# Performance work log

Measured on AMD Instinct MI355X. Metric: run time of the kernel, lower is better.

Reference implementation:

```python
import jax, jax.numpy as jnp
import numpy as np

N = 100_000   # nodes
E = 1_600_000 # edges (avg degree 16)
D = 128       # input_dim
H = 128       # hidden_dim
G = 64        # graphs in batch
C = 2         # num_classes


def setup_inputs() -> dict:
    key = jax.random.key(0)
    ks = jax.random.split(key, 16)
    x = jax.random.normal(ks[0], (N, D), dtype=jnp.float32)
    edge_index = jax.random.randint(ks[1], (2, E), 0, N, dtype=jnp.int32)
    batch = jnp.sort(jax.random.randint(ks[2], (N,), 0, G, dtype=jnp.int32))
    def lin(k, fin, fout):
        s = 1.0 / np.sqrt(fin)
        kw, kb = jax.random.split(k)
        W = jax.random.uniform(kw, (fin, fout), jnp.float32, -s, s)
        b = jax.random.uniform(kb, (fout,), jnp.float32, -s, s)
        return W, b
    W0, b0 = lin(ks[3], D, H)
    W1, b1 = lin(ks[4], H, H)
    W2, b2 = lin(ks[5], H, H)
    Wc1, bc1 = lin(ks[6], 2 * H, H)
    Wc2, bc2 = lin(ks[7], H, C)
    return dict(x=x, edge_index=edge_index, batch=batch,
                W0=W0, b0=b0, W1=W1, b1=b1, W2=W2, b2=b2,
                Wc1=Wc1, bc1=bc1, Wc2=Wc2, bc2=bc2)


def _gcn_layer(x, W, b, src, dst, dinv):
    # GCNConv with self-loops and symmetric normalization:
    # out_i = sum_{j->i} d_j^{-1/2} d_i^{-1/2} (x_j W) + d_i^{-1} (x_i W) + b
    h = x @ W                                   # [N, H]
    coef = dinv[src] * dinv[dst]                # [E]
    agg = jax.ops.segment_sum(h[src] * coef[:, None], dst, num_segments=N)
    return agg + h * (dinv * dinv)[:, None] + b


def reference(x, edge_index, batch, W0, b0, W1, b1, W2, b2, Wc1, bc1, Wc2, bc2):
    src, dst = edge_index[0], edge_index[1]
    # degree with self-loops (in-degree on target nodes + 1)
    deg = jax.ops.segment_sum(jnp.ones((E,), jnp.float32), dst, num_segments=N) + 1.0
    dinv = jax.lax.rsqrt(deg)
    for W, b in ((W0, b0), (W1, b1), (W2, b2)):
        x = jax.nn.relu(_gcn_layer(x, W, b, src, dst, dinv))
        # dropout: inference mode -> identity
    # global mean pool per graph
    sums = jax.ops.segment_sum(x, batch, num_segments=G)            # [G, H]
    cnt = jax.ops.segment_sum(jnp.ones((N,), jnp.float32), batch, num_segments=G)
    pooled = sums / jnp.maximum(cnt, 1.0)[:, None]
    combined = jnp.concatenate([pooled, pooled], axis=1)            # [G, 2H]
    hcls = jax.nn.relu(combined @ Wc1 + bc1)
    return hcls @ Wc2 + bc2                                         # [G, C]
```

## Files before the change

### kernel.cpp

```cpp
#include <hip/hip_runtime.h>

#define HDIM 128
#define GCOUNT 64
#define CHUNK 2048

__device__ __forceinline__ float bfl(unsigned u) { return __uint_as_float(u << 16); }
__device__ __forceinline__ float bfh(unsigned u) { return __uint_as_float(u & 0xffff0000u); }
__device__ __forceinline__ unsigned short f2bf(float f) {
  unsigned u = __float_as_uint(f);
  unsigned r = (u + 0x7fffu + ((u >> 16) & 1u)) >> 16;
  return (unsigned short)r;
}
__device__ __forceinline__ unsigned pk2(float a, float b) {
  return (unsigned)f2bf(a) | ((unsigned)f2bf(b) << 16);
}

typedef __attribute__((ext_vector_type(8))) short short8;
typedef __attribute__((ext_vector_type(4))) float f32x4;

__device__ __forceinline__ unsigned qb(float v, float rinv) {
  int q = (int)rintf(v * rinv);
  return (unsigned)(q & 0xff);
}


__global__ void mega1(const float* __restrict__ W0, const float* __restrict__ W1,
                      const float* __restrict__ W2,
                      unsigned short* __restrict__ h0, unsigned short* __restrict__ l0,
                      unsigned short* __restrict__ h1, unsigned short* __restrict__ l1,
                      unsigned short* __restrict__ h2, unsigned short* __restrict__ l2,
                      float* __restrict__ pooled, float* __restrict__ gcnt, int pz,
                      const int* __restrict__ dst, int E, int G, int NB1,
                      int* __restrict__ gcount,
                      const float* __restrict__ x, uint2* __restrict__ S,
                      float* __restrict__ cs_base, int n) {
  __shared__ int hist[512];
  int b = blockIdx.x, t = threadIdx.x;
  if (b < 192) {
    int w = b >> 6;
    int idx = (b & 63) * 256 + t;
    const float* W = (w == 0) ? W0 : (w == 1) ? W1 : W2;
    unsigned short* hi = (w == 0) ? h0 : (w == 1) ? h1 : h2;
    unsigned short* lo = (w == 0) ? l0 : (w == 1) ? l1 : l2;
    int k = idx >> 7, nn = idx & 127;
    float wv = W[idx];
    unsigned short h = f2bf(wv);
    float hf = __uint_as_float((unsigned)h << 16);
    unsigned short l = f2bf(wv - hf);
    hi[nn * 128 + k] = h;
    lo[nn * 128 + k] = l;
  } else if (b < 192 + pz) {
    int i = (b - 192) * 256 + t;
    if (i < GCOUNT * HDIM) pooled[i] = 0.f;
    else if (i - GCOUNT * HDIM < GCOUNT) gcnt[i - GCOUNT * HDIM] = 0.f;
  } else if (b < 192 + pz + G) {
    int blk = b - 192 - pz;
    for (int i = t; i < NB1; i += 256) hist[i] = 0;
    __syncthreads();
    int base = blk * CHUNK;
    #pragma unroll
    for (int j = 0; j < CHUNK / 256; j++) {
      int e = base + j * 256 + t;
      if (e < E) atomicAdd(&hist[dst[e] >> 8], 1);
    }
    __syncthreads();
    for (int i = t; i < NB1; i += 256) gcount[i * G + blk] = hist[i];
  } else {
    int idx = (b - 192 - pz - G) * 16 + (t >> 4);
    int l = t & 15;
    int ridx = min(idx, n - 1);
    float4 f0 = ((const float4*)x)[(size_t)ridx * 32 + l * 2];
    float4 f1 = ((const float4*)x)[(size_t)ridx * 32 + l * 2 + 1];
    float v0 = f0.x, v1 = f0.y, v2 = f0.z, v3 = f0.w;
    float v4 = f1.x, v5 = f1.y, v6 = f1.z, v7 = f1.w;
    float mx = fmaxf(fmaxf(fmaxf(fabsf(v0), fabsf(v1)), fmaxf(fabsf(v2), fabsf(v3))),
                     fmaxf(fmaxf(fabsf(v4), fabsf(v5)), fmaxf(fabsf(v6), fabsf(v7))));
    mx = fmaxf(mx, __shfl_xor(mx, 1));
    mx = fmaxf(mx, __shfl_xor(mx, 2));
    mx = fmaxf(mx, __shfl_xor(mx, 4));
    mx = fmaxf(mx, __shfl_xor(mx, 8));
    float c = mx * (1.0f / 127.0f);
    float rinv = (mx > 0.f) ? 127.0f / mx : 0.f;
    if (idx < n) {
      unsigned lo = qb(v0, rinv) | (qb(v1, rinv) << 8) | (qb(v2, rinv) << 16) | (qb(v3, rinv) << 24);
      unsigned hi = qb(v4, rinv) | (qb(v5, rinv) << 8) | (qb(v6, rinv) << 16) | (qb(v7, rinv) << 24);
      S[(size_t)idx * 16 + l] = make_uint2(lo, hi);
      if (l == 0) cs_base[idx] = c;
    }
  }
}


__global__ void scanA(int* __restrict__ g, int* __restrict__ bsum, int M) {
  __shared__ int sh[1024];
  int t = threadIdx.x;
  int i = blockIdx.x * 1024 + t;
  int v = (i < M) ? g[i] : 0;
  sh[t] = v;
  __syncthreads();
  for (int off = 1; off < 1024; off <<= 1) {
    int u = (t >= off) ? sh[t - off] : 0;
    __syncthreads();
    sh[t] += u;
    __syncthreads();
  }
  if (i < M) g[i] = sh[t] - v;
  if (t == 1023) bsum[blockIdx.x] = sh[1023];
}

__global__ void scanB(int* __restrict__ g, const int* __restrict__ bsum, int nb, int M) {
  __shared__ int sh[512];
  int t = threadIdx.x;
  if (t < 512) sh[t] = (t < nb) ? bsum[t] : 0;
  __syncthreads();
  for (int off = 1; off < 512; off <<= 1) {
    int u = (t < 512 && t >= off) ? sh[t - off] : 0;
    __syncthreads();
    if (t < 512) sh[t] += u;
    __syncthreads();
  }
  #pragma unroll
  for (int k = 0; k < 2; k++) {
    int i = blockIdx.x * 2048 + k * 1024 + t;
    if (i < M) {
      int j = i >> 10;
      if (j) g[i] += sh[j - 1];
    }
  }
}


__global__ void rs_scatter(const int* __restrict__ src, const int* __restrict__ dst,
                           const int* __restrict__ gscan, int E, int G, int NB1,
                           uint2* __restrict__ sp) {
  __shared__ int run[512];
  int blk = blockIdx.x, t = threadIdx.x;
  for (int i = t; i < NB1; i += 256) run[i] = gscan[i * G + blk];
  __syncthreads();
  int base = blk * CHUNK;
  #pragma unroll
  for (int j = 0; j < CHUNK / 256; j++) {
    int e = base + j * 256 + t;
    if (e < E) {
      int d = dst[e];
      int pos = atomicAdd(&run[d >> 8], 1);
      sp[pos] = make_uint2((unsigned)d, (unsigned)src[e]);
    }
  }
}


__global__ void csr_fine(const uint2* __restrict__ sp, const int* __restrict__ gscan,
                         int E, int G, int NB1,
                         int* __restrict__ rowp, int* __restrict__ colv,
                         float* __restrict__ dinv, const float* __restrict__ cs_base,
                         float* __restrict__ cs, int n) {
  __shared__ int hist[256];
  __shared__ int scn[256];
  __shared__ int run2[256];
  int hb = blockIdx.x, t = threadIdx.x;
  int O = gscan[hb * G];
  int Oe = (hb == NB1 - 1) ? E : gscan[(hb + 1) * G];
  if (t < 256) hist[t] = 0;
  __syncthreads();
  for (int e = O + t; e < Oe; e += 512) atomicAdd(&hist[sp[e].x & 255], 1);
  __syncthreads();
  int v = 0;
  if (t < 256) { v = hist[t]; scn[t] = v; }
  __syncthreads();
  for (int off = 1; off < 256; off <<= 1) {
    int u = (t < 256 && t >= off) ? scn[t - off] : 0;
    __syncthreads();
    if (t < 256) scn[t] += u;
    __syncthreads();
  }
  if (t < 256) {
    int excl = scn[t] - v;
    run2[t] = O + excl;
    int d = (hb << 8) + t;
    rowp[d] = O + excl;
    if (d < n) {
      float dv = rsqrtf((float)v + 1.0f);
      dinv[d] = dv;
      cs[d] = cs_base[d] * dv;
    }
  }
  if (hb == NB1 - 1 && t == 0) rowp[n] = E;
  __syncthreads();
  for (int e = O + t; e < Oe; e += 512) {
    uint2 p = sp[e];
    int pos = atomicAdd(&run2[p.x & 255], 1);
    colv[pos] = (int)p.y;
  }
}


__device__ __forceinline__ void acc8(uint2 v, float c, float* a) {
  int xx = (int)v.x, yy = (int)v.y;
  a[0] += c * (float)(signed char)(xx);
  a[1] += c * (float)(signed char)(xx >> 8);
  a[2] += c * (float)(signed char)(xx >> 16);
  a[3] += c * (float)(xx >> 24);
  a[4] += c * (float)(signed char)(yy);
  a[5] += c * (float)(signed char)(yy >> 8);
  a[6] += c * (float)(signed char)(yy >> 16);
  a[7] += c * (float)(yy >> 24);
}

__global__ void agg_i8(const uint2* __restrict__ S, const float* __restrict__ cs,
                       const float* __restrict__ dinv,
                       const int* __restrict__ rowp, const int* __restrict__ col,
                       uint4* __restrict__ OUT, int n) {
  int g = (blockIdx.x * blockDim.x + threadIdx.x) >> 4;
  int lane = threadIdx.x & 15;
  if (g >= n) return;
  float a[8];
  {
    uint2 q = S[(size_t)g * 16 + lane];
    float c = cs[g];
    int xx = (int)q.x, yy = (int)q.y;
    a[0] = c * (float)(signed char)(xx);
    a[1] = c * (float)(signed char)(xx >> 8);
    a[2] = c * (float)(signed char)(xx >> 16);
    a[3] = c * (float)(xx >> 24);
    a[4] = c * (float)(signed char)(yy);
    a[5] = c * (float)(signed char)(yy >> 8);
    a[6] = c * (float)(signed char)(yy >> 16);
    a[7] = c * (float)(yy >> 24);
  }
  int e0 = rowp[g], e1 = rowp[g + 1];
  int e = e0;
  for (; e + 7 < e1; e += 8) {
    int s0 = col[e],     s1 = col[e + 1], s2 = col[e + 2], s3 = col[e + 3];
    int s4 = col[e + 4], s5 = col[e + 5], s6 = col[e + 6], s7 = col[e + 7];
    uint2 q0 = S[(size_t)s0 * 16 + lane];
    uint2 q1 = S[(size_t)s1 * 16 + lane];
    uint2 q2 = S[(size_t)s2 * 16 + lane];
    uint2 q3 = S[(size_t)s3 * 16 + lane];
    uint2 q4 = S[(size_t)s4 * 16 + lane];
    uint2 q5 = S[(size_t)s5 * 16 + lane];
    uint2 q6 = S[(size_t)s6 * 16 + lane];
    uint2 q7 = S[(size_t)s7 * 16 + lane];
    float c0 = cs[s0], c1 = cs[s1], c2 = cs[s2], c3 = cs[s3];
    float c4 = cs[s4], c5 = cs[s5], c6 = cs[s6], c7 = cs[s7];
    acc8(q0, c0, a); acc8(q1, c1, a); acc8(q2, c2, a); acc8(q3, c3, a);
    acc8(q4, c4, a); acc8(q5, c5, a); acc8(q6, c6, a); acc8(q7, c7, a);
  }
  for (; e + 3 < e1; e += 4) {
    int s0 = col[e], s1 = col[e + 1], s2 = col[e + 2], s3 = col[e + 3];
    uint2 q0 = S[(size_t)s0 * 16 + lane];
    uint2 q1 = S[(size_t)s1 * 16 + lane];
    uint2 q2 = S[(size_t)s2 * 16 + lane];
    uint2 q3 = S[(size_t)s3 * 16 + lane];
    float c0 = cs[s0], c1 = cs[s1], c2 = cs[s2], c3 = cs[s3];
    acc8(q0, c0, a); acc8(q1, c1, a); acc8(q2, c2, a); acc8(q3, c3, a);
  }
  for (; e < e1; e++) {
    int s = col[e];
    uint2 q = S[(size_t)s * 16 + lane];
    acc8(q, cs[s], a);
  }
  float d = dinv[g];
  uint4 o;
  o.x = pk2(a[0] * d, a[1] * d); o.y = pk2(a[2] * d, a[3] * d);
  o.z = pk2(a[4] * d, a[5] * d); o.w = pk2(a[6] * d, a[7] * d);
  OUT[(size_t)g * 16 + lane] = o;
}


__global__ __launch_bounds__(256) void gemm_mfma_q8(
    const uint4* __restrict__ A, const uint4* __restrict__ WThi, const uint4* __restrict__ WTlo,
    const float* __restrict__ bias, const float* __restrict__ dinv,
    unsigned char* __restrict__ Sout, float* __restrict__ csout, int n) {
  __shared__ char smem[34816];
  __shared__ float Lc[64];
  uint4* Wl = (uint4*)smem;
  int t = threadIdx.x;
  int lane = t & 63, wv = t >> 6;
  int m = lane & 15, quad = lane >> 4;
  int block0 = blockIdx.x * 64;
  int arow = block0 + wv * 16 + m;
  uint4 av[4];
  #pragma unroll
  for (int kb = 0; kb < 4; kb++)
    av[kb] = (arow < n) ? A[(size_t)arow * 16 + kb * 4 + quad] : make_uint4(0, 0, 0, 0);
  f32x4 acc[8];
  #pragma unroll
  for (int i = 0; i < 8; i++) acc[i] = (f32x4){0.f, 0.f, 0.f, 0.f};

  #pragma unroll
  for (int i = 0; i < 8; i++) {
    int idx = t + i * 256;
    Wl[(idx >> 4) * 17 + (idx & 15)] = WThi[idx];
  }
  __syncthreads();
  #pragma unroll
  for (int kb = 0; kb < 4; kb++) {
    short8 af = __builtin_bit_cast(short8, av[kb]);
    #pragma unroll
    for (int nt = 0; nt < 8; nt++) {
      uint4 bh = Wl[(nt * 16 + m) * 17 + kb * 4 + quad];
      acc[nt] = __builtin_amdgcn_mfma_f32_16x16x32_bf16(af, __builtin_bit_cast(short8, bh), acc[nt], 0, 0, 0);
    }
  }
  __syncthreads();
  #pragma unroll
  for (int i = 0; i < 8; i++) {
    int idx = t + i * 256;
    Wl[(idx >> 4) * 17 + (idx & 15)] = WTlo[idx];
  }
  __syncthreads();
  #pragma unroll
  for (int kb = 0; kb < 4; kb++) {
    short8 af = __builtin_bit_cast(short8, av[kb]);
    #pragma unroll
    for (int nt = 0; nt < 8; nt++) {
      uint4 bl = Wl[(nt * 16 + m) * 17 + kb * 4 + quad];
      acc[nt] = __builtin_amdgcn_mfma_f32_16x16x32_bf16(af, __builtin_bit_cast(short8, bl), acc[nt], 0, 0, 0);
    }
  }
  __syncthreads();

  #pragma unroll
  for (int r = 0; r < 4; r++) {
    int lrow = wv * 16 + quad * 4 + r;
    int grow = block0 + lrow;
    float sc = (grow < n) ? dinv[grow] : 0.f;
    float v[8];
    float mx = 0.f;
    #pragma unroll
    for (int nt = 0; nt < 8; nt++) {
      v[nt] = fmaxf(acc[nt][r] + bias[nt * 16 + m], 0.f) * sc;
      mx = fmaxf(mx, v[nt]);
    }
    mx = fmaxf(mx, __shfl_xor(mx, 1));
    mx = fmaxf(mx, __shfl_xor(mx, 2));
    mx = fmaxf(mx, __shfl_xor(mx, 4));
    mx = fmaxf(mx, __shfl_xor(mx, 8));
    float c = mx * (1.0f / 127.0f);
    float rinv = (mx > 0.f) ? 127.0f / mx : 0.f;
    #pragma unroll
    for (int nt = 0; nt < 8; nt++) {
      smem[lrow * 144 + nt * 16 + m] = (char)(int)rintf(v[nt] * rinv);
    }
    if (m == 0) Lc[lrow] = c;
  }
  __syncthreads();
  for (int i = t; i < 512; i += 256) {
    int lrow = i >> 3, seg = i & 7;
    int grow = block0 + lrow;
    if (grow < n)
      ((uint4*)Sout)[(size_t)grow * 8 + seg] = *(const uint4*)&smem[lrow * 144 + seg * 16];
  }
  if (t < 64 && block0 + t < n) csout[block0 + t] = Lc[t];
}


__global__ __launch_bounds__(256) void gemm_mfma(
    const uint4* __restrict__ A, const uint4* __restrict__ WThi, const uint4* __restrict__ WTlo,
    const float* __restrict__ bias, unsigned short* __restrict__ Y, int n) {
  __shared__ char smem[34816];
  uint4* Wl = (uint4*)smem;
  int t = threadIdx.x;
  int lane = t & 63, wv = t >> 6;
  int m = lane & 15, quad = lane >> 4;
  int block0 = blockIdx.x * 64;
  int arow = block0 + wv * 16 + m;
  uint4 av[4];
  #pragma unroll
  for (int kb = 0; kb < 4; kb++)
    av[kb] = (arow < n) ? A[(size_t)arow * 16 + kb * 4 + quad] : make_uint4(0, 0, 0, 0);
  f32x4 acc[8];
  #pragma unroll
  for (int i = 0; i < 8; i++) acc[i] = (f32x4){0.f, 0.f, 0.f, 0.f};

  #pragma unroll
  for (int i = 0; i < 8; i++) {
    int idx = t + i * 256;
    Wl[(idx >> 4) * 17 + (idx & 15)] = WThi[idx];
  }
  __syncthreads();
  #pragma unroll
  for (int kb = 0; kb < 4; kb++) {
    short8 af = __builtin_bit_cast(short8, av[kb]);
    #pragma unroll
    for (int nt = 0; nt < 8; nt++) {
      uint4 bh = Wl[(nt * 16 + m) * 17 + kb * 4 + quad];
      acc[nt] = __builtin_amdgcn_mfma_f32_16x16x32_bf16(af, __builtin_bit_cast(short8, bh), acc[nt], 0, 0, 0);
    }
  }
  __syncthreads();
  #pragma unroll
  for (int i = 0; i < 8; i++) {
    int idx = t + i * 256;
    Wl[(idx >> 4) * 17 + (idx & 15)] = WTlo[idx];
  }
  __syncthreads();
  #pragma unroll
  for (int kb = 0; kb < 4; kb++) {
    short8 af = __builtin_bit_cast(short8, av[kb]);
    #pragma unroll
    for (int nt = 0; nt < 8; nt++) {
      uint4 bl = Wl[(nt * 16 + m) * 17 + kb * 4 + quad];
      acc[nt] = __builtin_amdgcn_mfma_f32_16x16x32_bf16(af, __builtin_bit_cast(short8, bl), acc[nt], 0, 0, 0);
    }
  }
  __syncthreads();

  unsigned short* Ls = (unsigned short*)smem;
  #pragma unroll
  for (int r = 0; r < 4; r++) {
    int lrow = wv * 16 + quad * 4 + r;
    #pragma unroll
    for (int nt = 0; nt < 8; nt++) {
      float v = fmaxf(acc[nt][r] + bias[nt * 16 + m], 0.f);
      Ls[lrow * 136 + nt * 16 + m] = f2bf(v);
    }
  }
  __syncthreads();
  for (int i = t; i < 1024; i += 256) {
    int lrow = i >> 4, seg = i & 15;
    int grow = block0 + lrow;
    if (grow < n)
      ((uint4*)Y)[(size_t)grow * 16 + seg] = *(const uint4*)&smem[lrow * 272 + seg * 16];
  }
}


__global__ void pool_kernel(const unsigned short* __restrict__ X, const int* __restrict__ batch,
                            float* __restrict__ pooled, float* __restrict__ gcnt, int n) {
  int t = threadIdx.x;
  int r0 = blockIdx.x * 64;
  if (r0 >= n) return;
  int r1 = min(r0 + 64, n);
  int g = batch[r0];
  float acc = 0.f, cl = 0.f;
  for (int r = r0; r < r1; r++) {
    int gr = batch[r];
    if (gr != g) {
      atomicAdd(&pooled[g * HDIM + t], acc);
      if (t == 0) atomicAdd(&gcnt[g], cl);
      acc = 0.f; cl = 0.f; g = gr;
    }
    acc += __uint_as_float((unsigned)X[(size_t)r * HDIM + t] << 16);
    cl += 1.f;
  }
  atomicAdd(&pooled[g * HDIM + t], acc);
  if (t == 0) atomicAdd(&gcnt[g], cl);
}


__global__ void cls_kernel(const float* __restrict__ pooled, const float* __restrict__ gcnt,
                           const float* __restrict__ Wc1, const float* __restrict__ bc1,
                           const float* __restrict__ Wc2, const float* __restrict__ bc2,
                           float* __restrict__ out) {
  __shared__ float p[HDIM];
  __shared__ float r0s[HDIM], r1s[HDIM];
  int g = blockIdx.x, t = threadIdx.x;
  float c = fmaxf(gcnt[g], 1.0f);
  p[t] = pooled[g * HDIM + t] / c;
  __syncthreads();
  float acc = bc1[t];
  for (int k = 0; k < HDIM; k++) {
    acc += p[k] * (Wc1[k * HDIM + t] + Wc1[(HDIM + k) * HDIM + t]);
  }
  float h = fmaxf(acc, 0.f);
  r0s[t] = h * Wc2[t * 2 + 0];
  r1s[t] = h * Wc2[t * 2 + 1];
  __syncthreads();
  for (int s2 = 64; s2 > 0; s2 >>= 1) {
    if (t < s2) { r0s[t] += r0s[t + s2]; r1s[t] += r1s[t + s2]; }
    __syncthreads();
  }
  if (t == 0) {
    out[g * 2 + 0] = r0s[0] + bc2[0];
    out[g * 2 + 1] = r1s[0] + bc2[1];
  }
}


extern "C" void kernel_launch(void* const* d_in, const int* in_sizes, int n_in,
                              void* d_out, int out_size, void* d_ws, size_t ws_size,
                              hipStream_t stream) {
  const float* x   = (const float*)d_in[0];
  const int*   ei  = (const int*)d_in[1];
  const int*   bat = (const int*)d_in[2];
  const float* W0  = (const float*)d_in[3];
  const float* b0  = (const float*)d_in[4];
  const float* W1  = (const float*)d_in[5];
  const float* b1  = (const float*)d_in[6];
  const float* W2  = (const float*)d_in[7];
  const float* b2  = (const float*)d_in[8];
  const float* Wc1 = (const float*)d_in[9];
  const float* bc1 = (const float*)d_in[10];
  const float* Wc2 = (const float*)d_in[11];
  const float* bc2 = (const float*)d_in[12];
  float* out = (float*)d_out;

  int N = in_sizes[0] / HDIM;
  int E = in_sizes[1] / 2;
  const int* src = ei;
  const int* dst = ei + E;

  int NB1 = (N + 255) >> 8;
  int G = (E + CHUNK - 1) / CHUNK;
  int M = NB1 * G;

  char* ws = (char*)d_ws;
  size_t off = 0;
  auto alloc = [&](size_t bytes) -> void* {
    void* p = (void*)(ws + off);
    off += (bytes + 511) & ~(size_t)511;
    return p;
  };
  unsigned char* Sa = (unsigned char*)alloc((size_t)N * HDIM * 2);
  unsigned char* Sb = Sa + (size_t)N * HDIM;
  unsigned short* H = (unsigned short*)Sa;
  unsigned short* Abuf = (unsigned short*)alloc((size_t)N * HDIM * 2);
  float* csa  = (float*)alloc((size_t)N * 4);
  float* csb  = (float*)alloc((size_t)N * 4);
  float* cs_base = (float*)alloc((size_t)N * 4);
  float* dinv = (float*)alloc((size_t)N * 4);
  int*   rowp = (int*)alloc((size_t)(NB1 * 256 + 2) * 4);
  int*   colv = (int*)alloc((size_t)E * 4);
  uint2* sp   = (uint2*)alloc((size_t)E * 8);
  float* pooled = (float*)alloc((size_t)GCOUNT * HDIM * 4);
  float* gcnt   = (float*)alloc((size_t)GCOUNT * 4);
  unsigned short* wt_hi[3], *wt_lo[3];
  for (int i = 0; i < 3; i++) {
    wt_hi[i] = (unsigned short*)alloc(HDIM * HDIM * 2);
    wt_lo[i] = (unsigned short*)alloc(HDIM * HDIM * 2);
  }
  int* gcount = (int*)alloc((size_t)(M + 2) * 4);
  int nbM = (M + 1023) / 1024;
  int* bsum = (int*)alloc((size_t)nbM * 4);

  int pz = (GCOUNT * HDIM + GCOUNT + 255) / 256;
  int psb = (N + 15) / 16;
  mega1<<<192 + pz + G + psb, 256, 0, stream>>>(W0, W1, W2,
      wt_hi[0], wt_lo[0], wt_hi[1], wt_lo[1], wt_hi[2], wt_lo[2],
      pooled, gcnt, pz, dst, E, G, NB1, gcount,
      x, (uint2*)Sa, cs_base, N);

  scanA<<<nbM, 1024, 0, stream>>>(gcount, bsum, M);
  scanB<<<(M + 2047) / 2048, 1024, 0, stream>>>(gcount, bsum, nbM, M);

  rs_scatter<<<G, 256, 0, stream>>>(src, dst, gcount, E, G, NB1, sp);
  csr_fine<<<NB1, 512, 0, stream>>>(sp, gcount, E, G, NB1, rowp, colv,
      dinv, cs_base, csa, N);

  int aggBlocks = (N + 15) / 16;
  int gemmBlocks = (N + 63) / 64;

  agg_i8<<<aggBlocks, 256, 0, stream>>>((const uint2*)Sa, csa, dinv, rowp, colv, (uint4*)Abuf, N);
  gemm_mfma_q8<<<gemmBlocks, 256, 0, stream>>>((const uint4*)Abuf, (const uint4*)wt_hi[0],
      (const uint4*)wt_lo[0], b0, dinv, Sb, csb, N);

  agg_i8<<<aggBlocks, 256, 0, stream>>>((const uint2*)Sb, csb, dinv, rowp, colv, (uint4*)Abuf, N);
  gemm_mfma_q8<<<gemmBlocks, 256, 0, stream>>>((const uint4*)Abuf, (const uint4*)wt_hi[1],
      (const uint4*)wt_lo[1], b1, dinv, Sa, csa, N);

  agg_i8<<<aggBlocks, 256, 0, stream>>>((const uint2*)Sa, csa, dinv, rowp, colv, (uint4*)Abuf, N);
  gemm_mfma<<<gemmBlocks, 256, 0, stream>>>((const uint4*)Abuf, (const uint4*)wt_hi[2],
      (const uint4*)wt_lo[2], b2, H, N);

  pool_kernel<<<(N + 63) / 64, 128, 0, stream>>>(H, bat, pooled, gcnt, N);
  cls_kernel<<<GCOUNT, HDIM, 0, stream>>>(pooled, gcnt, Wc1, bc1, Wc2, bc2, out);
}
```

Baseline: 378.7 us.

## Fuse int8 aggregation with MFMA GEMM and pooling into per-layer kernels

Each layer's int8 neighbour aggregation now runs inside the GEMM kernel. The aggregated bf16 tile goes straight into shared memory in MFMA operand layout, so the Abuf round-trip through global memory and one launch per layer are gone. The last layer also folds the mean-pool atomics into the epilogue instead of writing H and running a separate pool kernel. Blocks grow to 512 threads covering 128 rows with 64 KB of shared memory, and weight staging uses an MFMA-friendly layout overlapped with the aggregation. The cost is lower occupancy and less latency hiding for the gather-heavy aggregation, since each 16-lane group now handles 4 rows serially.

```diff
diff --git a/kernel.cpp b/kernel.cpp
--- a/kernel.cpp
+++ b/kernel.cpp
@@ -207,120 +207,135 @@
   a[7] += c * (float)(yy >> 24);
 }
 
-__global__ void agg_i8(const uint2* __restrict__ S, const float* __restrict__ cs,
-                       const float* __restrict__ dinv,
-                       const int* __restrict__ rowp, const int* __restrict__ col,
-                       uint4* __restrict__ OUT, int n) {
-  int g = (blockIdx.x * blockDim.x + threadIdx.x) >> 4;
-  int lane = threadIdx.x & 15;
-  if (g >= n) return;
-  float a[8];
-  {
-    uint2 q = S[(size_t)g * 16 + lane];
-    float c = cs[g];
-    int xx = (int)q.x, yy = (int)q.y;
-    a[0] = c * (float)(signed char)(xx);
-    a[1] = c * (float)(signed char)(xx >> 8);
-    a[2] = c * (float)(signed char)(xx >> 16);
-    a[3] = c * (float)(xx >> 24);
-    a[4] = c * (float)(signed char)(yy);
-    a[5] = c * (float)(signed char)(yy >> 8);
-    a[6] = c * (float)(signed char)(yy >> 16);
-    a[7] = c * (float)(yy >> 24);
-  }
-  int e0 = rowp[g], e1 = rowp[g + 1];
-  int e = e0;
-  for (; e + 7 < e1; e += 8) {
-    int s0 = col[e],     s1 = col[e + 1], s2 = col[e + 2], s3 = col[e + 3];
-    int s4 = col[e + 4], s5 = col[e + 5], s6 = col[e + 6], s7 = col[e + 7];
-    uint2 q0 = S[(size_t)s0 * 16 + lane];
-    uint2 q1 = S[(size_t)s1 * 16 + lane];
-    uint2 q2 = S[(size_t)s2 * 16 + lane];
-    uint2 q3 = S[(size_t)s3 * 16 + lane];
-    uint2 q4 = S[(size_t)s4 * 16 + lane];
-    uint2 q5 = S[(size_t)s5 * 16 + lane];
-    uint2 q6 = S[(size_t)s6 * 16 + lane];
-    uint2 q7 = S[(size_t)s7 * 16 + lane];
-    float c0 = cs[s0], c1 = cs[s1], c2 = cs[s2], c3 = cs[s3];
-    float c4 = cs[s4], c5 = cs[s5], c6 = cs[s6], c7 = cs[s7];
-    acc8(q0, c0, a); acc8(q1, c1, a); acc8(q2, c2, a); acc8(q3, c3, a);
-    acc8(q4, c4, a); acc8(q5, c5, a); acc8(q6, c6, a); acc8(q7, c7, a);
-  }
-  for (; e + 3 < e1; e += 4) {
-    int s0 = col[e], s1 = col[e + 1], s2 = col[e + 2], s3 = col[e + 3];
-    uint2 q0 = S[(size_t)s0 * 16 + lane];
-    uint2 q1 = S[(size_t)s1 * 16 + lane];
-    uint2 q2 = S[(size_t)s2 * 16 + lane];
-    uint2 q3 = S[(size_t)s3 * 16 + lane];
-    float c0 = cs[s0], c1 = cs[s1], c2 = cs[s2], c3 = cs[s3];
-    acc8(q0, c0, a); acc8(q1, c1, a); acc8(q2, c2, a); acc8(q3, c3, a);
-  }
-  for (; e < e1; e++) {
-    int s = col[e];
-    uint2 q = S[(size_t)s * 16 + lane];
-    acc8(q, cs[s], a);
-  }
-  float d = dinv[g];
-  uint4 o;
-  o.x = pk2(a[0] * d, a[1] * d); o.y = pk2(a[2] * d, a[3] * d);
-  o.z = pk2(a[4] * d, a[5] * d); o.w = pk2(a[6] * d, a[7] * d);
-  OUT[(size_t)g * 16 + lane] = o;
-}
-
-
-__global__ __launch_bounds__(256) void gemm_mfma_q8(
-    const uint4* __restrict__ A, const uint4* __restrict__ WThi, const uint4* __restrict__ WTlo,
-    const float* __restrict__ bias, const float* __restrict__ dinv,
+
+__device__ __forceinline__ void agg_phase(
+    const uint2* __restrict__ S, const float* __restrict__ cs,
+    const float* __restrict__ dinv,
+    const int* __restrict__ rowp, const int* __restrict__ col,
+    uint4* At, int block0, int t, int n) {
+  int grp = t >> 4, gl = t & 15;
+  #pragma unroll 1
+  for (int k = 0; k < 4; k++) {
+    int lrow = grp * 4 + k;
+    int g = block0 + lrow;
+    uint4 o = make_uint4(0u, 0u, 0u, 0u);
+    if (g < n) {
+      float a[8];
+      {
+        uint2 q = S[(size_t)g * 16 + gl];
+        float c = cs[g];
+        int xx = (int)q.x, yy = (int)q.y;
+        a[0] = c * (float)(signed char)(xx);
+        a[1] = c * (float)(signed char)(xx >> 8);
+        a[2] = c * (float)(signed char)(xx >> 16);
+        a[3] = c * (float)(xx >> 24);
+        a[4] = c * (float)(signed char)(yy);
+        a[5] = c * (float)(signed char)(yy >> 8);
+        a[6] = c * (float)(signed char)(yy >> 16);
+        a[7] = c * (float)(yy >> 24);
+      }
+      int e0 = rowp[g], e1 = rowp[g + 1];
+      int e = e0;
+      for (; e + 7 < e1; e += 8) {
+        int s0 = col[e],     s1 = col[e + 1], s2 = col[e + 2], s3 = col[e + 3];
+        int s4 = col[e + 4], s5 = col[e + 5], s6 = col[e + 6], s7 = col[e + 7];
+        uint2 q0 = S[(size_t)s0 * 16 + gl];
+        uint2 q1 = S[(size_t)s1 * 16 + gl];
+        uint2 q2 = S[(size_t)s2 * 16 + gl];
+        uint2 q3 = S[(size_t)s3 * 16 + gl];
+        uint2 q4 = S[(size_t)s4 * 16 + gl];
+        uint2 q5 = S[(size_t)s5 * 16 + gl];
+        uint2 q6 = S[(size_t)s6 * 16 + gl];
+        uint2 q7 = S[(size_t)s7 * 16 + gl];
+        float c0 = cs[s0], c1 = cs[s1], c2 = cs[s2], c3 = cs[s3];
+        float c4 = cs[s4], c5 = cs[s5], c6 = cs[s6], c7 = cs[s7];
+        acc8(q0, c0, a); acc8(q1, c1, a); acc8(q2, c2, a); acc8(q3, c3, a);
+        acc8(q4, c4, a); acc8(q5, c5, a); acc8(q6, c6, a); acc8(q7, c7, a);
+      }
+      for (; e + 3 < e1; e += 4) {
+        int s0 = col[e], s1 = col[e + 1], s2 = col[e + 2], s3 = col[e + 3];
+        uint2 q0 = S[(size_t)s0 * 16 + gl];
+        uint2 q1 = S[(size_t)s1 * 16 + gl];
+        uint2 q2 = S[(size_t)s2 * 16 + gl];
+        uint2 q3 = S[(size_t)s3 * 16 + gl];
+        float c0 = cs[s0], c1 = cs[s1], c2 = cs[s2], c3 = cs[s3];
+        acc8(q0, c0, a); acc8(q1, c1, a); acc8(q2, c2, a); acc8(q3, c3, a);
+      }
+      for (; e < e1; e++) {
+        int s = col[e];
+        uint2 q = S[(size_t)s * 16 + gl];
+        acc8(q, cs[s], a);
+      }
+      float d = dinv[g];
+      o.x = pk2(a[0] * d, a[1] * d);
+      o.y = pk2(a[2] * d, a[3] * d);
+      o.z = pk2(a[4] * d, a[5] * d);
+      o.w = pk2(a[6] * d, a[7] * d);
+    }
+    At[((lrow >> 4) * 4 + (gl >> 2)) * 64 + (gl & 3) * 16 + (lrow & 15)] = o;
+  }
+}
+
+__device__ __forceinline__ void stage_w(uint4* Wl, const uint4* __restrict__ WT, int t) {
+  #pragma unroll
+  for (int i = 0; i < 4; i++) {
+    int idx = t + i * 512;
+    int nn = idx >> 4, cc = idx & 15;
+    Wl[((cc >> 2) * 8 + (nn >> 4)) * 64 + (cc & 3) * 16 + (nn & 15)] = WT[idx];
+  }
+}
+
+__global__ __launch_bounds__(512, 4) void fused_q8(
+    const uint2* __restrict__ S, const float* __restrict__ cs,
+    const float* __restrict__ dinv,
+    const int* __restrict__ rowp, const int* __restrict__ col,
+    const uint4* __restrict__ WThi, const uint4* __restrict__ WTlo,
+    const float* __restrict__ bias,
     unsigned char* __restrict__ Sout, float* __restrict__ csout, int n) {
-  __shared__ char smem[34816];
-  __shared__ float Lc[64];
+  __shared__ __align__(16) char smem[65536];
   uint4* Wl = (uint4*)smem;
+  uint4* At = (uint4*)(smem + 32768);
   int t = threadIdx.x;
   int lane = t & 63, wv = t >> 6;
   int m = lane & 15, quad = lane >> 4;
-  int block0 = blockIdx.x * 64;
-  int arow = block0 + wv * 16 + m;
+  int block0 = blockIdx.x * 128;
+
+  stage_w(Wl, WThi, t);
+  agg_phase(S, cs, dinv, rowp, col, At, block0, t, n);
+  __syncthreads();
+
   uint4 av[4];
   #pragma unroll
-  for (int kb = 0; kb < 4; kb++)
-    av[kb] = (arow < n) ? A[(size_t)arow * 16 + kb * 4 + quad] : make_uint4(0, 0, 0, 0);
+  for (int kb = 0; kb < 4; kb++) av[kb] = At[(wv * 4 + kb) * 64 + lane];
   f32x4 acc[8];
   #pragma unroll
   for (int i = 0; i < 8; i++) acc[i] = (f32x4){0.f, 0.f, 0.f, 0.f};
 
-  #pragma unroll
-  for (int i = 0; i < 8; i++) {
-    int idx = t + i * 256;
-    Wl[(idx >> 4) * 17 + (idx & 15)] = WThi[idx];
-  }
-  __syncthreads();
   #pragma unroll
   for (int kb = 0; kb < 4; kb++) {
     short8 af = __builtin_bit_cast(short8, av[kb]);
     #pragma unroll
     for (int nt = 0; nt < 8; nt++) {
-      uint4 bh = Wl[(nt * 16 + m) * 17 + kb * 4 + quad];
+      uint4 bh = Wl[(kb * 8 + nt) * 64 + lane];
       acc[nt] = __builtin_amdgcn_mfma_f32_16x16x32_bf16(af, __builtin_bit_cast(short8, bh), acc[nt], 0, 0, 0);
     }
   }
   __syncthreads();
-  #pragma unroll
-  for (int i = 0; i < 8; i++) {
-    int idx = t + i * 256;
-    Wl[(idx >> 4) * 17 + (idx & 15)] = WTlo[idx];
-  }
+  stage_w(Wl, WTlo, t);
   __syncthreads();
   #pragma unroll
   for (int kb = 0; kb < 4; kb++) {
     short8 af = __builtin_bit_cast(short8, av[kb]);
     #pragma unroll
     for (int nt = 0; nt < 8; nt++) {
-      uint4 bl = Wl[(nt * 16 + m) * 17 + kb * 4 + quad];
+      uint4 bl = Wl[(kb * 8 + nt) * 64 + lane];
       acc[nt] = __builtin_amdgcn_mfma_f32_16x16x32_bf16(af, __builtin_bit_cast(short8, bl), acc[nt], 0, 0, 0);
     }
   }
   __syncthreads();
 
+  char* stg = smem;
+  float* LcA = (float*)(smem + 18432);
   #pragma unroll
   for (int r = 0; r < 4; r++) {
     int lrow = wv * 16 + quad * 4 + r;
@@ -341,67 +356,64 @@
     float rinv = (mx > 0.f) ? 127.0f / mx : 0.f;
     #pragma unroll
     for (int nt = 0; nt < 8; nt++) {
-      smem[lrow * 144 + nt * 16 + m] = (char)(int)rintf(v[nt] * rinv);
-    }
-    if (m == 0) Lc[lrow] = c;
-  }
-  __syncthreads();
-  for (int i = t; i < 512; i += 256) {
+      stg[lrow * 144 + nt * 16 + m] = (char)(int)rintf(v[nt] * rinv);
+    }
+    if (m == 0) LcA[lrow] = c;
+  }
+  __syncthreads();
+  for (int i = t; i < 1024; i += 512) {
     int lrow = i >> 3, seg = i & 7;
     int grow = block0 + lrow;
     if (grow < n)
-      ((uint4*)Sout)[(size_t)grow * 8 + seg] = *(const uint4*)&smem[lrow * 144 + seg * 16];
-  }
-  if (t < 64 && block0 + t < n) csout[block0 + t] = Lc[t];
-}
-
-
-__global__ __launch_bounds__(256) void gemm_mfma(
-    const uint4* __restrict__ A, const uint4* __restrict__ WThi, const uint4* __restrict__ WTlo,
-    const float* __restrict__ bias, unsigned short* __restrict__ Y, int n) {
-  __shared__ char smem[34816];
+      ((uint4*)Sout)[(size_t)grow * 8 + seg] = *(const uint4*)&stg[lrow * 144 + seg * 16];
+  }
+  if (t < 128 && block0 + t < n) csout[block0 + t] = LcA[t];
+}
+
+__global__ __launch_bounds__(512, 4) void fused_final(
+    const uint2* __restrict__ S, const float* __restrict__ cs,
+    const float* __restrict__ dinv,
+    const int* __restrict__ rowp, const int* __restrict__ col,
+    const uint4* __restrict__ WThi, const uint4* __restrict__ WTlo,
+    const float* __restrict__ bias, const int* __restrict__ batch,
+    float* __restrict__ pooled, float* __restrict__ gcnt, int n) {
+  __shared__ __align__(16) char smem[65536];
   uint4* Wl = (uint4*)smem;
+  uint4* At = (uint4*)(smem + 32768);
   int t = threadIdx.x;
   int lane = t & 63, wv = t >> 6;
   int m = lane & 15, quad = lane >> 4;
-  int block0 = blockIdx.x * 64;
-  int arow = block0 + wv * 16 + m;
+  int block0 = blockIdx.x * 128;
+
+  stage_w(Wl, WThi, t);
+  agg_phase(S, cs, dinv, rowp, col, At, block0, t, n);
+  __syncthreads();
+
   uint4 av[4];
   #pragma unroll
-  for (int kb = 0; kb < 4; kb++)
-    av[kb] = (arow < n) ? A[(size_t)arow * 16 + kb * 4 + quad] : make_uint4(0, 0, 0, 0);
+  for (int kb = 0; kb < 4; kb++) av[kb] = At[(wv * 4 + kb) * 64 + lane];
   f32x4 acc[8];
   #pragma unroll
   for (int i = 0; i < 8; i++) acc[i] = (f32x4){0.f, 0.f, 0.f, 0.f};
 
-  #pragma unroll
-  for (int i = 0; i < 8; i++) {
-    int idx = t + i * 256;
-    Wl[(idx >> 4) * 17 + (idx & 15)] = WThi[idx];
-  }
-  __syncthreads();
   #pragma unroll
   for (int kb = 0; kb < 4; kb++) {
     short8 af = __builtin_bit_cast(short8, av[kb]);
     #pragma unroll
     for (int nt = 0; nt < 8; nt++) {
-      uint4 bh = Wl[(nt * 16 + m) * 17 + kb * 4 + quad];
+      uint4 bh = Wl[(kb * 8 + nt) * 64 + lane];
       acc[nt] = __builtin_amdgcn_mfma_f32_16x16x32_bf16(af, __builtin_bit_cast(short8, bh), acc[nt], 0, 0, 0);
     }
   }
   __syncthreads();
-  #pragma unroll
-  for (int i = 0; i < 8; i++) {
-    int idx = t + i * 256;
-    Wl[(idx >> 4) * 17 + (idx & 15)] = WTlo[idx];
-  }
+  stage_w(Wl, WTlo, t);
   __syncthreads();
   #pragma unroll
   for (int kb = 0; kb < 4; kb++) {
     short8 af = __builtin_bit_cast(short8, av[kb]);
     #pragma unroll
     for (int nt = 0; nt < 8; nt++) {
-      uint4 bl = Wl[(nt * 16 + m) * 17 + kb * 4 + quad];
+      uint4 bl = Wl[(kb * 8 + nt) * 64 + lane];
       acc[nt] = __builtin_amdgcn_mfma_f32_16x16x32_bf16(af, __builtin_bit_cast(short8, bl), acc[nt], 0, 0, 0);
     }
   }
@@ -414,39 +426,32 @@
     #pragma unroll
     for (int nt = 0; nt < 8; nt++) {
       float v = fmaxf(acc[nt][r] + bias[nt * 16 + m], 0.f);
-      Ls[lrow * 136 + nt * 16 + m] = f2bf(v);
-    }
-  }
-  __syncthreads();
-  for (int i = t; i < 1024; i += 256) {
-    int lrow = i >> 4, seg = i & 15;
-    int grow = block0 + lrow;
-    if (grow < n)
-      ((uint4*)Y)[(size_t)grow * 16 + seg] = *(const uint4*)&smem[lrow * 272 + seg * 16];
-  }
-}
-
-
-__global__ void pool_kernel(const unsigned short* __restrict__ X, const int* __restrict__ batch,
-                            float* __restrict__ pooled, float* __restrict__ gcnt, int n) {
-  int t = threadIdx.x;
-  int r0 = blockIdx.x * 64;
-  if (r0 >= n) return;
-  int r1 = min(r0 + 64, n);
-  int g = batch[r0];
-  float acc = 0.f, cl = 0.f;
-  for (int r = r0; r < r1; r++) {
-    int gr = batch[r];
-    if (gr != g) {
-      atomicAdd(&pooled[g * HDIM + t], acc);
-      if (t == 0) atomicAdd(&gcnt[g], cl);
-      acc = 0.f; cl = 0.f; g = gr;
-    }
-    acc += __uint_as_float((unsigned)X[(size_t)r * HDIM + t] << 16);
-    cl += 1.f;
-  }
-  atomicAdd(&pooled[g * HDIM + t], acc);
-  if (t == 0) atomicAdd(&gcnt[g], cl);
+      Ls[lrow * 128 + nt * 16 + m] = f2bf(v);
+    }
+  }
+  __syncthreads();
+  if (t < 128) {
+    float a2 = 0.f, cl = 0.f;
+    int gcur = -1;
+    for (int r = 0; r < 128; r++) {
+      int grow = block0 + r;
+      if (grow >= n) break;
+      int gr = batch[grow];
+      if (gr != gcur) {
+        if (gcur >= 0) {
+          atomicAdd(&pooled[gcur * HDIM + t], a2);
+          if (t == 0) atomicAdd(&gcnt[gcur], cl);
+        }
+        a2 = 0.f; cl = 0.f; gcur = gr;
+      }
+      a2 += bfl((unsigned)Ls[r * 128 + t]);
+      cl += 1.f;
+    }
+    if (gcur >= 0) {
+      atomicAdd(&pooled[gcur * HDIM + t], a2);
+      if (t == 0) atomicAdd(&gcnt[gcur], cl);
+    }
+  }
 }
 
 
@@ -515,8 +520,6 @@
   };
   unsigned char* Sa = (unsigned char*)alloc((size_t)N * HDIM * 2);
   unsigned char* Sb = Sa + (size_t)N * HDIM;
-  unsigned short* H = (unsigned short*)Sa;
-  unsigned short* Abuf = (unsigned short*)alloc((size_t)N * HDIM * 2);
   float* csa  = (float*)alloc((size_t)N * 4);
   float* csb  = (float*)alloc((size_t)N * 4);
   float* cs_base = (float*)alloc((size_t)N * 4);
@@ -549,21 +552,16 @@
   csr_fine<<<NB1, 512, 0, stream>>>(sp, gcount, E, G, NB1, rowp, colv,
       dinv, cs_base, csa, N);
 
-  int aggBlocks = (N + 15) / 16;
-  int gemmBlocks = (N + 63) / 64;
-
-  agg_i8<<<aggBlocks, 256, 0, stream>>>((const uint2*)Sa, csa, dinv, rowp, colv, (uint4*)Abuf, N);
-  gemm_mfma_q8<<<gemmBlocks, 256, 0, stream>>>((const uint4*)Abuf, (const uint4*)wt_hi[0],
-      (const uint4*)wt_lo[0], b0, dinv, Sb, csb, N);
-
-  agg_i8<<<aggBlocks, 256, 0, stream>>>((const uint2*)Sb, csb, dinv, rowp, colv, (uint4*)Abuf, N);
-  gemm_mfma_q8<<<gemmBlocks, 256, 0, stream>>>((const uint4*)Abuf, (const uint4*)wt_hi[1],
-      (const uint4*)wt_lo[1], b1, dinv, Sa, csa, N);
-
-  agg_i8<<<aggBlocks, 256, 0, stream>>>((const uint2*)Sa, csa, dinv, rowp, colv, (uint4*)Abuf, N);
-  gemm_mfma<<<gemmBlocks, 256, 0, stream>>>((const uint4*)Abuf, (const uint4*)wt_hi[2],
-      (const uint4*)wt_lo[2], b2, H, N);
-
-  pool_kernel<<<(N + 63) / 64, 128, 0, stream>>>(H, bat, pooled, gcnt, N);
+  int fusedBlocks = (N + 127) / 128;
+
+  fused_q8<<<fusedBlocks, 512, 0, stream>>>((const uint2*)Sa, csa, dinv, rowp, colv,
+      (const uint4*)wt_hi[0], (const uint4*)wt_lo[0], b0, Sb, csb, N);
+
+  fused_q8<<<fusedBlocks, 512, 0, stream>>>((const uint2*)Sb, csb, dinv, rowp, colv,
+      (const uint4*)wt_hi[1], (const uint4*)wt_lo[1], b1, Sa, csa, N);
+
+  fused_final<<<fusedBlocks, 512, 0, stream>>>((const uint2*)Sa, csa, dinv, rowp, colv,
+      (const uint4*)wt_hi[2], (const uint4*)wt_lo[2], b2, bat, pooled, gcnt, N);
+
   cls_kernel<<<GCOUNT, HDIM, 0, stream>>>(pooled, gcnt, Wc1, bc1, Wc2, bc2, out);
 }
```

Result: slower. 398.8 us (+5.3%).
